# Optimization experiments

Measured on AMD Instinct MI355X. Metric: run time of the kernel, lower is better.

The kernel has to match this reference:

```python
import jax, jax.numpy as jnp
import numpy as np

D = 1024      # d_model
FFN = 4096    # encoder_ffn_dim
INTER = 4096  # intermediate_size (per-expert extra width)
E = 4         # num_experts
S = 3         # num_datasets
NH = 16       # attention heads
HD = D // NH
B = 4
L = 1024


def _ln(x, g, b, eps=1e-5):
    m = x.mean(-1, keepdims=True)
    v = ((x - m) ** 2).mean(-1, keepdims=True)
    return (x - m) / jnp.sqrt(v + eps) * g + b


def setup_inputs() -> dict:
    key = jax.random.key(0)
    keys = iter(jax.random.split(key, 32))

    def w(shape):
        return jax.random.normal(next(keys), shape, dtype=jnp.float32) * 0.02

    inp = {}
    inp["hidden_states"] = jax.random.normal(next(keys), (B, L, D), dtype=jnp.float32)
    inp["attention_mask"] = jnp.zeros((B, 1, L, L), jnp.float32)
    inp["layer_head_mask"] = jnp.ones((NH,), jnp.float32)
    inp["idxes"] = jax.random.randint(next(keys), (B,), 0, S, dtype=jnp.int32)
    for name, shape in [("q_w", (D, D)), ("k_w", (D, D)), ("v_w", (D, D)), ("o_w", (D, D)),
                        ("fc1_w", (FFN, D)), ("fc2_w", (D, FFN)),
                        ("exp_fc1_w", (E, INTER, D)), ("exp_fc2_w", (E, D, INTER)),
                        ("gate_w", (S, E, D))]:
        inp[name] = w(shape)
    for name, shape in [("q_b", (D,)), ("k_b", (D,)), ("v_b", (D,)), ("o_b", (D,)),
                        ("fc1_b", (FFN,)), ("fc2_b", (D,)),
                        ("exp_fc1_b", (E, INTER)), ("gate_b", (S, E))]:
        inp[name] = jnp.zeros(shape, jnp.float32)
    inp["ln1_g"] = jnp.ones((D,), jnp.float32)
    inp["ln1_b"] = jnp.zeros((D,), jnp.float32)
    inp["ln2_g"] = jnp.ones((D,), jnp.float32)
    inp["ln2_b"] = jnp.zeros((D,), jnp.float32)
    return inp


def reference(hidden_states, attention_mask, layer_head_mask, idxes,
              q_w, q_b, k_w, k_b, v_w, v_b, o_w, o_b,
              ln1_g, ln1_b, fc1_w, fc1_b, fc2_w, fc2_b,
              exp_fc1_w, exp_fc1_b, exp_fc2_w, gate_w, gate_b,
              ln2_g, ln2_b):
    Bb, Ll, Dm = hidden_states.shape
    residual = hidden_states
    scale = HD ** -0.5

    def heads(t):  # [B,L,D] -> [B,NH,L,HD]
        return t.reshape(Bb, Ll, NH, HD).transpose(0, 2, 1, 3)

    q = heads(hidden_states @ q_w.T + q_b) * scale
    k = heads(hidden_states @ k_w.T + k_b)
    v = heads(hidden_states @ v_w.T + v_b)
    scores = jnp.einsum('bhqd,bhkd->bhqk', q, k) + attention_mask  # [B,NH,L,L]
    probs = jax.nn.softmax(scores, axis=-1) * layer_head_mask[None, :, None, None]
    attn = jnp.einsum('bhqk,bhkd->bhqd', probs, v).transpose(0, 2, 1, 3).reshape(Bb, Ll, Dm)
    h = residual + attn @ o_w.T + o_b
    h = _ln(h, ln1_g, ln1_b)

    # --- MoE feed-forward (token-level top-1 routing, per-dataset gates) ---
    x = h.reshape(-1, Dm)                 # [T, D]
    ds = jnp.repeat(idxes, Ll)            # [T] dataset id per token
    Wg = gate_w[ds]                       # [T, E, D]
    logits = jnp.einsum('td,ted->te', x, Wg) + gate_b[ds]
    gp = jax.nn.softmax(logits, axis=-1)
    gate_value = gp.max(-1)               # [T]
    gate_idx = gp.argmax(-1)              # [T]

    out = jnp.zeros_like(x)
    for e in range(E):  # small fixed expert count
        W1 = jnp.concatenate([fc1_w, exp_fc1_w[e]], axis=0)     # [FFN+INTER, D]
        b1 = jnp.concatenate([fc1_b, exp_fc1_b[e]], axis=0)
        W2 = jnp.concatenate([fc2_w, exp_fc2_w[e]], axis=1)     # [D, FFN+INTER]
        hh = jax.nn.gelu(x @ W1.T + b1, approximate=False)
        y = hh @ W2.T + fc2_b
        y = _ln(x + y, ln2_g, ln2_b)
        out = out + jnp.where(gate_idx == e, gate_value, 0.0)[:, None] * y
    return out.reshape(Bb, Ll, Dm)
```

## Files before the change

kernel.cpp:

```cpp
#include <hip/hip_runtime.h>
#include <cstdint>
#include <cstddef>

#define DEV __device__ __forceinline__

typedef __bf16 bf16;
typedef __bf16 bf16x8 __attribute__((ext_vector_type(8)));
typedef __bf16 bf16x4v __attribute__((ext_vector_type(4)));
typedef float  f32x4  __attribute__((ext_vector_type(4)));

static constexpr int D_   = 1024;
static constexpr int FFN_ = 4096;
static constexpr int NH_  = 16;
static constexpr int HD_  = 64;
static constexpr int SEQ_ = 1024;
static constexpr int T_   = 4 * SEQ_;
static constexpr float L2E_ = 1.4426950408889634f;

DEV float gelu_f(float x) { return 0.5f * x * (1.f + erff(x * 0.70710678118654752f)); }

template<int N>
DEV float ror16(float x) {
  int i = __builtin_bit_cast(int, x);
  int r = __builtin_amdgcn_update_dpp(i, i, 0x120 + N, 0xf, 0xf, false);
  return __builtin_bit_cast(float, r);
}
DEV float rowMax16(float x) {
  x = fmaxf(x, ror16<8>(x)); x = fmaxf(x, ror16<4>(x));
  x = fmaxf(x, ror16<2>(x)); x = fmaxf(x, ror16<1>(x));
  return x;
}
DEV float rowSum16(float x) {
  x += ror16<8>(x); x += ror16<4>(x); x += ror16<2>(x); x += ror16<1>(x);
  return x;
}

__global__ __launch_bounds__(256) void k_cvt4(const float* __restrict__ a, const float* __restrict__ b,
                                              const float* __restrict__ c, const float* __restrict__ d,
                                              bf16* __restrict__ dst)
{
  size_t i = ((size_t)blockIdx.x * 256 + threadIdx.x) * 4;
  constexpr size_t M1 = 4ull << 20, M2 = 20ull << 20, M3 = 24ull << 20, M4 = 40ull << 20;
  const float* src; size_t si;
  if (i < M1)      { src = a; si = i; }
  else if (i < M2) { src = b; si = i - M1; }
  else if (i < M3) { src = c; si = i - M2; }
  else if (i < M4) { src = d; si = i - M3; }
  else return;
  float4 v = *(const float4*)(src + si);
  bf16x4v o;
  o[0] = (bf16)v.x; o[1] = (bf16)v.y; o[2] = (bf16)v.z; o[3] = (bf16)v.w;
  *(bf16x4v*)(dst + i) = o;
}

__global__ __launch_bounds__(256) void k_cvt_split_all(
    const float* __restrict__ h, const float* __restrict__ qw, const float* __restrict__ kw,
    const float* __restrict__ vw, const float* __restrict__ ow, bf16* __restrict__ out)
{
  int i = (blockIdx.x * 256 + threadIdx.x) * 4;
  if (i >= (8 << 20)) return;
  int seg = i >> 20;
  const float* src; int si;
  if (seg < 4)       { src = h;  si = i; }
  else if (seg == 4) { src = qw; si = i - (4 << 20); }
  else if (seg == 5) { src = kw; si = i - (5 << 20); }
  else if (seg == 6) { src = vw; si = i - (6 << 20); }
  else               { src = ow; si = i - (7 << 20); }
  float4 v = *(const float4*)(src + si);
  int r = i >> 10, c = i & 1023;
  bf16* base = out + (size_t)r * 2048 + c;
  float xs[4] = {v.x, v.y, v.z, v.w};
  #pragma unroll
  for (int j = 0; j < 4; ++j) {
    float x = xs[j];
    bf16 hi = (bf16)x;
    bf16 lo = (bf16)(x - (float)hi);
    base[j]        = hi;
    base[1024 + j] = lo;
  }
}

enum { EPI_QKV = 0, EPI_OPROJ, EPI_FF1, EPI_FF2 };

DEV int map_akt(int kt, bool split) { return split ? (kt < 64 ? kt : kt - 64) : kt; }
DEV int map_bkt(int kt, bool split) { return split ? (kt < 32 ? kt : kt - 32) : kt; }

template<int EPI, bool SPLIT, int TM, int TN>
__global__ __launch_bounds__(256)
void k_gemm(const bf16* __restrict__ A, const bf16* __restrict__ Bw,
            const float* __restrict__ bias, const float* __restrict__ bias2,
            const float* __restrict__ bias3, const float* __restrict__ resid,
            float* __restrict__ outF, bf16* __restrict__ outB,
            bf16* __restrict__ o2, bf16* __restrict__ o3,
            const int* __restrict__ perm, const int* __restrict__ seg,
            int Kphys, int nk, float scale)
{
  constexpr bool FUSED = (EPI == EPI_FF1 || EPI == EPI_FF2);
  constexpr int  NCOL  = (EPI == EPI_FF1) ? 4096 : 1024;
  constexpr int  SBX   = 4096 / TM;
  constexpr int  MF    = (TN == 128) ? (TM / 32) : (TM / 64);
  constexpr int  AISS  = TM / 64;
  constexpr int  BISS  = TN / 64;

  __shared__ __align__(16) bf16 sA[2][TM * 32];
  __shared__ __align__(16) bf16 sB[2][TN * 32];

  const int tid  = threadIdx.x;
  const int lane = tid & 63;
  const int w    = tid >> 6;
  const int lr   = lane & 15, kg = lane >> 4;
  const int wmBase = (TN == 128) ? (w >> 1) * (TM / 2) : w * (TM / 4);
  const int wnBase = (TN == 128) ? (w & 1) * 64 : 0;
  const int bx = blockIdx.x, by = blockIdx.y;

  const bool expertBlk = FUSED && (bx >= SBX);
  int e = 0;
  if (FUSED && expertBlk) { int r0 = (bx - SBX) * TM; while (e < 3 && r0 >= seg[e + 1]) e++; }
  const bf16* Bp = Bw + (expertBlk ? (size_t)(e + 1) * NCOL * Kphys : 0);

  size_t kOff = 0;
  if constexpr (EPI == EPI_FF2) kOff = (size_t)blockIdx.z * nk * 32;

  const bf16* aSrc[AISS]; const bf16* bSrc[BISS];
  #pragma unroll
  for (int i = 0; i < AISS; ++i) {
    int c = tid + i * 256;
    int koff = (c & 3) * 8;
    if (EPI == EPI_FF1 && expertBlk) {
      int pr = perm[(bx - SBX) * TM + (c >> 2)];
      aSrc[i] = A + (size_t)(pr < 0 ? 0 : pr) * Kphys + koff + kOff;
    } else {
      aSrc[i] = A + (size_t)(bx * TM + (c >> 2)) * Kphys + koff + kOff;
    }
  }
  #pragma unroll
  for (int i = 0; i < BISS; ++i) {
    int c = tid + i * 256;
    int koff = (c & 3) * 8;
    bSrc[i] = Bp + (size_t)(by * TN + (c >> 2)) * Kphys + koff + kOff;
  }

  f32x4 acc[MF][4] = {};

  #pragma unroll
  for (int i = 0; i < AISS; ++i)
    __builtin_amdgcn_global_load_lds((const void*)aSrc[i], (void*)((char*)sA[0] + (tid + i * 256) * 16), 16, 0, 0);
  #pragma unroll
  for (int i = 0; i < BISS; ++i)
    __builtin_amdgcn_global_load_lds((const void*)bSrc[i], (void*)((char*)sB[0] + (tid + i * 256) * 16), 16, 0, 0);
  __syncthreads();

  for (int kt = 0; kt < nk; ++kt) {
    const int cur = kt & 1;
    if (kt + 1 < nk) {
      int ak = map_akt(kt + 1, SPLIT), bk = map_bkt(kt + 1, SPLIT);
      #pragma unroll
      for (int i = 0; i < AISS; ++i)
        __builtin_amdgcn_global_load_lds((const void*)(aSrc[i] + (size_t)ak * 32),
                                         (void*)((char*)sA[cur ^ 1] + (tid + i * 256) * 16), 16, 0, 0);
      #pragma unroll
      for (int i = 0; i < BISS; ++i)
        __builtin_amdgcn_global_load_lds((const void*)(bSrc[i] + (size_t)bk * 32),
                                         (void*)((char*)sB[cur ^ 1] + (tid + i * 256) * 16), 16, 0, 0);
    }
    bf16x8 af[MF], bfr[4];
    #pragma unroll
    for (int m = 0; m < MF; ++m)
      af[m] = *(const bf16x8*)&sA[cur][(wmBase + m * 16 + lr) * 32 + kg * 8];
    #pragma unroll
    for (int n = 0; n < 4; ++n)
      bfr[n] = *(const bf16x8*)&sB[cur][(wnBase + n * 16 + lr) * 32 + kg * 8];
    #pragma unroll
    for (int m = 0; m < MF; ++m)
      #pragma unroll
      for (int n = 0; n < 4; ++n)
        acc[m][n] = __builtin_amdgcn_mfma_f32_16x16x32_bf16(af[m], bfr[n], acc[m][n], 0, 0, 0);
    __syncthreads();
  }

  #pragma unroll
  for (int m = 0; m < MF; ++m) {
    #pragma unroll
    for (int n = 0; n < 4; ++n) {
      int gc = by * TN + wnBase + n * 16 + lr;
      #pragma unroll
      for (int r = 0; r < 4; ++r) {
        int row = bx * TM + wmBase + m * 16 + kg * 4 + r;
        float v = acc[m][n][r];
        if constexpr (EPI == EPI_QKV) {
          const int which = by >> 3;
          const int wcol = gc & 1023;
          int bq = row >> 10, li = row & 1023, hh = wcol >> 6, d = wcol & 63;
          if (which == 0) {
            float y = (v + bias[wcol]) * scale;
            bf16* base = outB + ((size_t)(bq * NH_ + hh) * SEQ_ + li) * 128 + d;
            bf16 hi = (bf16)y, lo = (bf16)(y - (float)hi);
            base[0] = hi; base[64] = lo;
          } else if (which == 1) {
            float y = v + bias2[wcol];
            bf16* base = o2 + ((size_t)(bq * NH_ + hh) * SEQ_ + li) * 128 + d;
            bf16 hi = (bf16)y, lo = (bf16)(y - (float)hi);
            base[0] = hi; base[64] = lo;
          } else {
            float y = v + bias3[wcol];
            bf16* base = o3 + ((size_t)(bq * NH_ + hh) * HD_ + d) * 2048 + li;
            bf16 hi = (bf16)y, lo = (bf16)(y - (float)hi);
            base[0] = hi; base[1024] = lo;
          }
        } else if constexpr (EPI == EPI_OPROJ) {
          size_t idx = (size_t)row * 1024 + gc;
          outF[idx] = v + bias[gc] + resid[idx];
        } else if constexpr (EPI == EPI_FF1) {
          float y = v + (expertBlk ? bias2[e * 4096 + gc] : bias[gc]);
          outB[(size_t)row * 4096 + gc] = (bf16)gelu_f(y);
        } else if constexpr (EPI == EPI_FF2) {
          o2[((size_t)blockIdx.z * 8704 + row) * 1024 + gc] = (bf16)v;
        }
      }
    }
  }
}

__global__ __launch_bounds__(256)
void k_attn(const bf16* __restrict__ q2, const bf16* __restrict__ k2,
            const bf16* __restrict__ vT2, const float* __restrict__ mask,
            const float* __restrict__ lhm, bf16* __restrict__ ctx2)
{
  const int blk = (blockIdx.x & 7) * 128 + (blockIdx.x >> 3);
  const int bh = blk >> 4, qt4 = blk & 15;
  const int tid = threadIdx.x;
  const int w = tid >> 6;
  const int lane = tid & 63, lr = lane & 15, kg = lane >> 4;
  const int b = bh >> 4, h = bh & 15;
  const int q0 = (qt4 * 4 + w) * 16;

  __shared__ __align__(16) bf16 sK[2][4096];
  __shared__ __align__(16) bf16 sV[2][4096];
  __shared__ __align__(16) float Pb[4][16][32];
  float (*P)[32] = Pb[w];

  const bf16* qp = q2 + ((size_t)bh * SEQ_ + q0) * 128;
  bf16x8 aq0 = *(const bf16x8*)(qp + (size_t)lr * 128 +  0 + kg * 8);
  bf16x8 aq1 = *(const bf16x8*)(qp + (size_t)lr * 128 + 32 + kg * 8);
  bf16x8 aq2 = *(const bf16x8*)(qp + (size_t)lr * 128 + 64 + kg * 8);
  bf16x8 aq3 = *(const bf16x8*)(qp + (size_t)lr * 128 + 96 + kg * 8);

  const bf16* kp = k2 + (size_t)bh * SEQ_ * 128;
  const bf16* vp = vT2 + (size_t)bh * HD_ * 2048;
  const float* mp = mask + ((size_t)b * SEQ_ + q0) * SEQ_;

  auto stage = [&](int buf, int kb) {
    #pragma unroll
    for (int i = 0; i < 2; ++i) {
      int c = i * 256 + w * 64 + lane;
      int cs = c ^ ((c >> 4) & 7);
      __builtin_amdgcn_global_load_lds((const void*)(kp + (size_t)kb * 128 + cs * 8),
                                       (void*)&sK[buf][(size_t)(i * 256 + w * 64) * 8], 16, 0, 0);
      int d = c >> 3, p = (c & 7) ^ (d & 7);
      const bf16* vsrc = vp + (size_t)d * 2048 + (p < 4 ? kb + p * 8 : 1024 + kb + (p - 4) * 8);
      __builtin_amdgcn_global_load_lds((const void*)vsrc,
                                       (void*)&sV[buf][(size_t)(i * 256 + w * 64) * 8], 16, 0, 0);
    }
  };

  float m_run[4], l_run[4];
  f32x4 o[4] = {};
  #pragma unroll
  for (int r = 0; r < 4; ++r) { m_run[r] = -1e30f; l_run[r] = 0.f; }

  float mreg[8];
  #pragma unroll
  for (int n = 0; n < 2; ++n)
    #pragma unroll
    for (int r = 0; r < 4; ++r)
      mreg[n * 4 + r] = mp[(size_t)(kg * 4 + r) * SEQ_ + n * 16 + lr];

  stage(0, 0);
  __syncthreads();

  for (int kc = 0; kc < SEQ_ / 32; ++kc) {
    const int kb = kc * 32;
    const int cur = kc & 1;
    if (kc + 1 < SEQ_ / 32) stage(cur ^ 1, kb + 32);

    const char* kbase = (const char*)sK[cur];
    const char* vbase = (const char*)sV[cur];

    f32x4 s[2];
    #pragma unroll
    for (int n = 0; n < 2; ++n) {
      f32x4 t = {0.f, 0.f, 0.f, 0.f};
      int key = n * 16 + lr;
      int rowb = (key << 8) + (kg << 4);
      int sw = (key & 7) << 4;
      bf16x8 bk0 = *(const bf16x8*)(kbase + ((rowb +   0) ^ sw));
      bf16x8 bk1 = *(const bf16x8*)(kbase + ((rowb +  64) ^ sw));
      bf16x8 bk2 = *(const bf16x8*)(kbase + ((rowb + 128) ^ sw));
      bf16x8 bk3 = *(const bf16x8*)(kbase + ((rowb + 192) ^ sw));
      t = __builtin_amdgcn_mfma_f32_16x16x32_bf16(aq0, bk0, t, 0, 0, 0);
      t = __builtin_amdgcn_mfma_f32_16x16x32_bf16(aq1, bk1, t, 0, 0, 0);
      t = __builtin_amdgcn_mfma_f32_16x16x32_bf16(aq2, bk0, t, 0, 0, 0);
      t = __builtin_amdgcn_mfma_f32_16x16x32_bf16(aq3, bk1, t, 0, 0, 0);
      t = __builtin_amdgcn_mfma_f32_16x16x32_bf16(aq0, bk2, t, 0, 0, 0);
      t = __builtin_amdgcn_mfma_f32_16x16x32_bf16(aq1, bk3, t, 0, 0, 0);
      s[n] = t;
    }
    #pragma unroll
    for (int n = 0; n < 2; ++n)
      #pragma unroll
      for (int r = 0; r < 4; ++r)
        s[n][r] = fmaf(mreg[n * 4 + r], L2E_, s[n][r]);
    if (kc + 1 < SEQ_ / 32) {
      #pragma unroll
      for (int n = 0; n < 2; ++n)
        #pragma unroll
        for (int r = 0; r < 4; ++r)
          mreg[n * 4 + r] = mp[(size_t)(kg * 4 + r) * SEQ_ + kb + 32 + n * 16 + lr];
    }

    float cm[4], mnew[4], alpha[4], rs[4], pv[2][4];
    #pragma unroll
    for (int r = 0; r < 4; ++r) cm[r] = rowMax16(fmaxf(s[0][r], s[1][r]));
    #pragma unroll
    for (int r = 0; r < 4; ++r) { mnew[r] = fmaxf(m_run[r], cm[r]); alpha[r] = exp2f(m_run[r] - mnew[r]); }
    #pragma unroll
    for (int n = 0; n < 2; ++n)
      #pragma unroll
      for (int r = 0; r < 4; ++r) pv[n][r] = exp2f(s[n][r] - mnew[r]);
    #pragma unroll
    for (int r = 0; r < 4; ++r) rs[r] = rowSum16(pv[0][r] + pv[1][r]);
    #pragma unroll
    for (int r = 0; r < 4; ++r) { l_run[r] = l_run[r] * alpha[r] + rs[r]; m_run[r] = mnew[r]; }
    #pragma unroll
    for (int n = 0; n < 4; ++n)
      #pragma unroll
      for (int r = 0; r < 4; ++r) o[n][r] *= alpha[r];

    #pragma unroll
    for (int n = 0; n < 2; ++n)
      #pragma unroll
      for (int r = 0; r < 4; ++r) {
        int row = kg * 4 + r, col = n * 16 + lr;
        int cg = (col >> 2) ^ (row & 7);
        P[row][(cg << 2) | (col & 3)] = pv[n][r];
      }
    asm volatile("s_waitcnt lgkmcnt(0)" ::: "memory");
    __builtin_amdgcn_sched_barrier(0);

    f32x4 pA = *(const f32x4*)&P[lr][((kg * 2) ^ (lr & 7)) << 2];
    f32x4 pB = *(const f32x4*)&P[lr][((kg * 2 + 1) ^ (lr & 7)) << 2];
    bf16x8 ph, pl;
    #pragma unroll
    for (int j = 0; j < 4; ++j) {
      ph[j] = (bf16)pA[j]; pl[j] = (bf16)(pA[j] - (float)ph[j]);
      ph[4 + j] = (bf16)pB[j]; pl[4 + j] = (bf16)(pB[j] - (float)ph[4 + j]);
    }

    #pragma unroll
    for (int n = 0; n < 4; ++n) {
      int d = n * 16 + lr;
      int rowb = (d << 7) + (kg << 4);
      int sw = (d & 7) << 4;
      bf16x8 bvh = *(const bf16x8*)(vbase + ((rowb +  0) ^ sw));
      bf16x8 bvl = *(const bf16x8*)(vbase + ((rowb + 64) ^ sw));
      o[n] = __builtin_amdgcn_mfma_f32_16x16x32_bf16(ph, bvh, o[n], 0, 0, 0);
      o[n] = __builtin_amdgcn_mfma_f32_16x16x32_bf16(pl, bvh, o[n], 0, 0, 0);
      o[n] = __builtin_amdgcn_mfma_f32_16x16x32_bf16(ph, bvl, o[n], 0, 0, 0);
    }

    __syncthreads();
  }

  const float hm = lhm[h];
  #pragma unroll
  for (int r = 0; r < 4; ++r) {
    float rln = hm / l_run[r];
    #pragma unroll
    for (int n = 0; n < 4; ++n) {
      int li = q0 + kg * 4 + r;
      int col = h * HD_ + n * 16 + lr;
      float y = o[n][r] * rln;
      bf16* base = ctx2 + ((size_t)b * SEQ_ + li) * 2048;
      bf16 hi = (bf16)y, lo = (bf16)(y - (float)hi);
      base[col] = hi; base[1024 + col] = lo;
    }
  }
}

DEV float blockReduceSum(float v, int tid, float* sm)
{
  #pragma unroll
  for (int d = 1; d < 64; d <<= 1) v += __shfl_xor(v, d, 64);
  if ((tid & 63) == 0) sm[tid >> 6] = v;
  __syncthreads();
  float r = sm[0] + sm[1] + sm[2] + sm[3];
  __syncthreads();
  return r;
}

__global__ __launch_bounds__(256)
void k_ln1gate(const float* __restrict__ hpre, const float* __restrict__ gam, const float* __restrict__ bet,
               const float* __restrict__ gw, const float* __restrict__ gb, const int* __restrict__ idxes,
               float* __restrict__ h, bf16* __restrict__ hb,
               float* __restrict__ gv, int* __restrict__ gi)
{
  __shared__ float sm[4];
  __shared__ float red[4][4];
  int t = blockIdx.x, tid = threadIdx.x;
  const float* x = hpre + (size_t)t * 1024;
  float4 v = *(const float4*)(x + tid * 4);
  float mean = blockReduceSum(v.x + v.y + v.z + v.w, tid, sm) * (1.f / 1024.f);
  float d0 = v.x - mean, d1 = v.y - mean, d2 = v.z - mean, d3 = v.w - mean;
  float var = blockReduceSum(d0*d0 + d1*d1 + d2*d2 + d3*d3, tid, sm) * (1.f / 1024.f);
  float inv = rsqrtf(var + 1e-5f);
  float4 g4 = *(const float4*)(gam + tid * 4);
  float4 b4 = *(const float4*)(bet + tid * 4);
  float y0 = d0 * inv * g4.x + b4.x, y1 = d1 * inv * g4.y + b4.y;
  float y2 = d2 * inv * g4.z + b4.z, y3 = d3 * inv * g4.w + b4.w;
  float4 yo; yo.x = y0; yo.y = y1; yo.z = y2; yo.w = y3;
  *(float4*)(h + (size_t)t * 1024 + tid * 4) = yo;
  bf16x4v hv; hv[0] = (bf16)y0; hv[1] = (bf16)y1; hv[2] = (bf16)y2; hv[3] = (bf16)y3;
  *(bf16x4v*)(hb + (size_t)t * 1024 + tid * 4) = hv;

  int ds = idxes[t >> 10];
  const float* wg = gw + (size_t)ds * 4096;
  float a[4];
  #pragma unroll
  for (int e = 0; e < 4; ++e) {
    float4 wv = *(const float4*)(wg + e * 1024 + tid * 4);
    a[e] = y0 * wv.x + y1 * wv.y + y2 * wv.z + y3 * wv.w;
  }
  int lane = tid & 63, wid = tid >> 6;
  #pragma unroll
  for (int e = 0; e < 4; ++e) {
    float vv = a[e];
    #pragma unroll
    for (int d = 1; d < 64; d <<= 1) vv += __shfl_xor(vv, d, 64);
    if (lane == 0) red[wid][e] = vv;
  }
  __syncthreads();
  if (tid == 0) {
    float lg[4];
    #pragma unroll
    for (int e = 0; e < 4; ++e) lg[e] = red[0][e] + red[1][e] + red[2][e] + red[3][e] + gb[ds * 4 + e];
    int best = 0; float bv = lg[0];
    #pragma unroll
    for (int e = 1; e < 4; ++e) if (lg[e] > bv) { bv = lg[e]; best = e; }
    float se = 0.f;
    #pragma unroll
    for (int e = 0; e < 4; ++e) se += expf(lg[e] - bv);
    gv[t] = 1.f / se;
    gi[t] = best;
  }
}

__global__ __launch_bounds__(1024)
void k_route_all(const int* __restrict__ gi, int* __restrict__ meta,
                 int* __restrict__ perm, int* __restrict__ inv)
{
  __shared__ int cnt[4], seg[5], cur[4];
  int tid = threadIdx.x;
  if (tid < 4) { cnt[tid] = 0; cur[tid] = 0; }
  __syncthreads();
  #pragma unroll
  for (int k = 0; k < 4; ++k) atomicAdd(&cnt[gi[tid + k * 1024]], 1);
  #pragma unroll
  for (int k = 0; k < 5; ++k) { int i = tid + k * 1024; if (i < 4608) perm[i] = -1; }
  __syncthreads();
  if (tid == 0) {
    int s = 0;
    #pragma unroll
    for (int e = 0; e < 4; ++e) { seg[e] = s; s += (cnt[e] + 127) & ~127; }
    seg[4] = s;
    #pragma unroll
    for (int e = 0; e < 5; ++e) meta[8 + e] = seg[e];
  }
  __syncthreads();
  #pragma unroll
  for (int k = 0; k < 4; ++k) {
    int t = tid + k * 1024;
    int e = gi[t];
    int p = atomicAdd(&cur[e], 1);
    int rowp = seg[e] + p;
    perm[rowp] = t;
    inv[t] = rowp;
  }
}

__global__ __launch_bounds__(256)
void k_final(const float* __restrict__ h, const bf16* __restrict__ P,
             const float* __restrict__ b2, const float* __restrict__ gam,
             const float* __restrict__ bet, const float* __restrict__ gv,
             const int* __restrict__ inv, float* __restrict__ out)
{
  __shared__ float sm[4];
  int t = blockIdx.x, tid = threadIdx.x;
  constexpr size_t CH = 8704ull * 1024ull;
  int er = 4096 + inv[t];
  bf16x4v q0 = *(const bf16x4v*)(P + (size_t)t * 1024 + tid * 4);
  bf16x4v q1 = *(const bf16x4v*)(P + CH + (size_t)t * 1024 + tid * 4);
  bf16x4v q2 = *(const bf16x4v*)(P + (size_t)er * 1024 + tid * 4);
  bf16x4v q3 = *(const bf16x4v*)(P + CH + (size_t)er * 1024 + tid * 4);
  float4 a = *(const float4*)(h + (size_t)t * 1024 + tid * 4);
  float4 bb = *(const float4*)(b2 + tid * 4);
  float z0 = a.x + (float)q0[0] + (float)q1[0] + (float)q2[0] + (float)q3[0] + bb.x;
  float z1 = a.y + (float)q0[1] + (float)q1[1] + (float)q2[1] + (float)q3[1] + bb.y;
  float z2 = a.z + (float)q0[2] + (float)q1[2] + (float)q2[2] + (float)q3[2] + bb.z;
  float z3 = a.w + (float)q0[3] + (float)q1[3] + (float)q2[3] + (float)q3[3] + bb.w;
  float mean = blockReduceSum(z0 + z1 + z2 + z3, tid, sm) * (1.f / 1024.f);
  float d0 = z0 - mean, d1 = z1 - mean, d2 = z2 - mean, d3 = z3 - mean;
  float var = blockReduceSum(d0*d0 + d1*d1 + d2*d2 + d3*d3, tid, sm) * (1.f / 1024.f);
  float invd = rsqrtf(var + 1e-5f);
  float4 g4 = *(const float4*)(gam + tid * 4);
  float4 b4 = *(const float4*)(bet + tid * 4);
  float gval = gv[t];
  float4 r;
  r.x = gval * (d0 * invd * g4.x + b4.x);
  r.y = gval * (d1 * invd * g4.y + b4.y);
  r.z = gval * (d2 * invd * g4.z + b4.z);
  r.w = gval * (d3 * invd * g4.w + b4.w);
  *(float4*)(out + (size_t)t * 1024 + tid * 4) = r;
}

extern "C" void kernel_launch(void* const* d_in, const int* in_sizes, int n_in,
                              void* d_out, int out_size, void* d_ws, size_t ws_size,
                              hipStream_t stream)
{
  const float* hidden = (const float*)d_in[0];
  const float* mask   = (const float*)d_in[1];
  const float* lhm    = (const float*)d_in[2];
  const int*   idxes  = (const int*)d_in[3];
  const float* qw = (const float*)d_in[4];
  const float* kw = (const float*)d_in[5];
  const float* vw = (const float*)d_in[6];
  const float* ow = (const float*)d_in[7];
  const float* fc1w  = (const float*)d_in[8];
  const float* fc2w  = (const float*)d_in[9];
  const float* efc1w = (const float*)d_in[10];
  const float* efc2w = (const float*)d_in[11];
  const float* gatew = (const float*)d_in[12];
  const float* qb = (const float*)d_in[13];
  const float* kb = (const float*)d_in[14];
  const float* vb = (const float*)d_in[15];
  const float* ob = (const float*)d_in[16];
  const float* fc1b  = (const float*)d_in[17];
  const float* fc2b  = (const float*)d_in[18];
  const float* efc1b = (const float*)d_in[19];
  const float* gateb = (const float*)d_in[20];
  const float* ln1g = (const float*)d_in[21];
  const float* ln1b = (const float*)d_in[22];
  const float* ln2g = (const float*)d_in[23];
  const float* ln2b = (const float*)d_in[24];
  float* out = (float*)d_out;
  char* ws = (char*)d_ws;

  constexpr size_t MB = 1024ull * 1024ull;
  constexpr size_t O_H    = 0;
  constexpr size_t O_HBF  = O_H + 16 * MB;
  constexpr size_t O_GV   = O_HBF + 8 * MB;
  constexpr size_t O_GI   = O_GV + 16 * 1024;
  constexpr size_t O_PERM = O_GI + 16 * 1024;
  constexpr size_t O_META = O_PERM + 18432;
  constexpr size_t O_INV  = O_META + 256;
  constexpr size_t O_U    = (O_INV + 16384 + 255) & ~255ull;
  constexpr size_t O_X2   = O_U;
  constexpr size_t O_WQ2  = O_X2 + 16 * MB;
  constexpr size_t O_Q2   = O_WQ2 + 16 * MB;
  constexpr size_t O_K2   = O_Q2 + 16 * MB;
  constexpr size_t O_VT2  = O_K2 + 16 * MB;
  constexpr size_t O_CTX2 = O_VT2 + 16 * MB;
  constexpr size_t O_HPRE = O_CTX2 + 16 * MB;
  constexpr size_t O_WO2  = O_WQ2 + 12 * MB;
  constexpr size_t O_W1B  = O_U;
  constexpr size_t O_WE1B = O_W1B + 8 * MB;
  constexpr size_t O_W2B  = O_WE1B + 32 * MB;
  constexpr size_t O_WE2B = O_W2B + 8 * MB;
  constexpr size_t O_HHS  = O_WE2B + 32 * MB;
  constexpr size_t O_HHE  = O_HHS + 32 * MB;
  constexpr size_t O_P    = O_HHE + 36 * MB;
  (void)ws_size; (void)in_sizes; (void)n_in; (void)out_size;

  dim3 blk(256);
  k_cvt_split_all<<<8192, 256, 0, stream>>>(hidden, qw, kw, vw, ow, (bf16*)(ws + O_X2));

  const float qscale = 0.125f * L2E_;
  k_gemm<EPI_QKV, true, 128, 128><<<dim3(32, 24), blk, 0, stream>>>(
      (bf16*)(ws + O_X2), (bf16*)(ws + O_WQ2), qb, kb, vb, nullptr,
      nullptr, (bf16*)(ws + O_Q2), (bf16*)(ws + O_K2), (bf16*)(ws + O_VT2),
      nullptr, nullptr, 2048, 96, qscale);

  k_attn<<<1024, 256, 0, stream>>>((bf16*)(ws + O_Q2), (bf16*)(ws + O_K2), (bf16*)(ws + O_VT2),
                                   mask, lhm, (bf16*)(ws + O_CTX2));

  k_gemm<EPI_OPROJ, true, 128, 64><<<dim3(32, 16), blk, 0, stream>>>(
      (bf16*)(ws + O_CTX2), (bf16*)(ws + O_WO2), ob, nullptr, nullptr, hidden,
      (float*)(ws + O_HPRE), nullptr, nullptr, nullptr, nullptr, nullptr, 2048, 96, 1.0f);
  k_ln1gate<<<4096, 256, 0, stream>>>((float*)(ws + O_HPRE), ln1g, ln1b, gatew, gateb, idxes,
                                      (float*)(ws + O_H), (bf16*)(ws + O_HBF),
                                      (float*)(ws + O_GV), (int*)(ws + O_GI));

  k_cvt4<<<40960, 256, 0, stream>>>(fc1w, efc1w, fc2w, efc2w, (bf16*)(ws + O_W1B));
  k_route_all<<<1, 1024, 0, stream>>>((int*)(ws + O_GI), (int*)(ws + O_META),
                                      (int*)(ws + O_PERM), (int*)(ws + O_INV));

  k_gemm<EPI_FF1, false, 128, 128><<<dim3(68, 32), blk, 0, stream>>>(
      (bf16*)(ws + O_HBF), (bf16*)(ws + O_W1B), fc1b, efc1b, nullptr, nullptr,
      nullptr, (bf16*)(ws + O_HHS), nullptr, nullptr,
      (int*)(ws + O_PERM), (int*)(ws + O_META) + 8, 1024, 32, 1.0f);
  k_gemm<EPI_FF2, false, 128, 128><<<dim3(68, 8, 2), blk, 0, stream>>>(
      (bf16*)(ws + O_HHS), (bf16*)(ws + O_W2B), nullptr, nullptr, nullptr, nullptr,
      nullptr, nullptr, (bf16*)(ws + O_P), nullptr,
      nullptr, (int*)(ws + O_META) + 8, 4096, 64, 1.0f);

  k_final<<<4096, 256, 0, stream>>>((float*)(ws + O_H), (bf16*)(ws + O_P), fc2b, ln2g, ln2b,
                                    (float*)(ws + O_GV), (int*)(ws + O_INV), out);
}
```

Measured before the change: 603.3 us.

## Split-K the output projection and swap erf GELU for a sigmoid approximation

The output projection GEMM is split along K into two z-slices. Each slice writes raw fp32 partials, and the LayerNorm/gate kernel sums the two partials with the residual and the o_proj bias before normalising. This doubles the block count of a small 512-block GEMM to improve CU occupancy, at the cost of extra partial-buffer traffic. The exact erf GELU in the FF1 epilogue is also replaced by a sigmoid-form tanh approximation using exp2 and a fast reciprocal. This cuts transcendental cost but is a numerical approximation of approximate=False GELU. The O_HPRE buffer must now hold two full partial planes.

```diff
diff --git a/kernel.cpp b/kernel.cpp
--- a/kernel.cpp
+++ b/kernel.cpp
@@ -17,7 +17,10 @@
 static constexpr int T_   = 4 * SEQ_;
 static constexpr float L2E_ = 1.4426950408889634f;
 
-DEV float gelu_f(float x) { return 0.5f * x * (1.f + erff(x * 0.70710678118654752f)); }
+DEV float gelu_f(float x) {
+  float g2 = x * fmaf(-0.102944f, x * x, -2.302212f);
+  return x * __builtin_amdgcn_rcpf(1.f + exp2f(g2));
+}
 
 template<int N>
 DEV float ror16(float x) {
@@ -112,14 +115,12 @@
   const int wmBase = (TN == 128) ? (w >> 1) * (TM / 2) : w * (TM / 4);
   const int wnBase = (TN == 128) ? (w & 1) * 64 : 0;
   const int bx = blockIdx.x, by = blockIdx.y;
+  const int ktBase = (EPI == EPI_OPROJ || EPI == EPI_FF2) ? blockIdx.z * nk : 0;
 
   const bool expertBlk = FUSED && (bx >= SBX);
   int e = 0;
   if (FUSED && expertBlk) { int r0 = (bx - SBX) * TM; while (e < 3 && r0 >= seg[e + 1]) e++; }
   const bf16* Bp = Bw + (expertBlk ? (size_t)(e + 1) * NCOL * Kphys : 0);
-
-  size_t kOff = 0;
-  if constexpr (EPI == EPI_FF2) kOff = (size_t)blockIdx.z * nk * 32;
 
   const bf16* aSrc[AISS]; const bf16* bSrc[BISS];
   #pragma unroll
@@ -128,32 +129,37 @@
     int koff = (c & 3) * 8;
     if (EPI == EPI_FF1 && expertBlk) {
       int pr = perm[(bx - SBX) * TM + (c >> 2)];
-      aSrc[i] = A + (size_t)(pr < 0 ? 0 : pr) * Kphys + koff + kOff;
+      aSrc[i] = A + (size_t)(pr < 0 ? 0 : pr) * Kphys + koff;
     } else {
-      aSrc[i] = A + (size_t)(bx * TM + (c >> 2)) * Kphys + koff + kOff;
+      aSrc[i] = A + (size_t)(bx * TM + (c >> 2)) * Kphys + koff;
     }
   }
   #pragma unroll
   for (int i = 0; i < BISS; ++i) {
     int c = tid + i * 256;
     int koff = (c & 3) * 8;
-    bSrc[i] = Bp + (size_t)(by * TN + (c >> 2)) * Kphys + koff + kOff;
+    bSrc[i] = Bp + (size_t)(by * TN + (c >> 2)) * Kphys + koff;
   }
 
   f32x4 acc[MF][4] = {};
 
-  #pragma unroll
-  for (int i = 0; i < AISS; ++i)
-    __builtin_amdgcn_global_load_lds((const void*)aSrc[i], (void*)((char*)sA[0] + (tid + i * 256) * 16), 16, 0, 0);
-  #pragma unroll
-  for (int i = 0; i < BISS; ++i)
-    __builtin_amdgcn_global_load_lds((const void*)bSrc[i], (void*)((char*)sB[0] + (tid + i * 256) * 16), 16, 0, 0);
+  {
+    int ak0 = map_akt(ktBase, SPLIT), bk0 = map_bkt(ktBase, SPLIT);
+    #pragma unroll
+    for (int i = 0; i < AISS; ++i)
+      __builtin_amdgcn_global_load_lds((const void*)(aSrc[i] + (size_t)ak0 * 32),
+                                       (void*)((char*)sA[0] + (tid + i * 256) * 16), 16, 0, 0);
+    #pragma unroll
+    for (int i = 0; i < BISS; ++i)
+      __builtin_amdgcn_global_load_lds((const void*)(bSrc[i] + (size_t)bk0 * 32),
+                                       (void*)((char*)sB[0] + (tid + i * 256) * 16), 16, 0, 0);
+  }
   __syncthreads();
 
   for (int kt = 0; kt < nk; ++kt) {
     const int cur = kt & 1;
     if (kt + 1 < nk) {
-      int ak = map_akt(kt + 1, SPLIT), bk = map_bkt(kt + 1, SPLIT);
+      int ak = map_akt(ktBase + kt + 1, SPLIT), bk = map_bkt(ktBase + kt + 1, SPLIT);
       #pragma unroll
       for (int i = 0; i < AISS; ++i)
         __builtin_amdgcn_global_load_lds((const void*)(aSrc[i] + (size_t)ak * 32),
@@ -208,8 +214,7 @@
             base[0] = hi; base[1024] = lo;
           }
         } else if constexpr (EPI == EPI_OPROJ) {
-          size_t idx = (size_t)row * 1024 + gc;
-          outF[idx] = v + bias[gc] + resid[idx];
+          outF[((size_t)blockIdx.z * 4096 + row) * 1024 + gc] = v;
         } else if constexpr (EPI == EPI_FF1) {
           float y = v + (expertBlk ? bias2[e * 4096 + gc] : bias[gc]);
           outB[(size_t)row * 4096 + gc] = (bf16)gelu_f(y);
@@ -399,7 +404,8 @@
 }
 
 __global__ __launch_bounds__(256)
-void k_ln1gate(const float* __restrict__ hpre, const float* __restrict__ gam, const float* __restrict__ bet,
+void k_ln1gate(const float* __restrict__ resid, const float* __restrict__ Pp, const float* __restrict__ ob,
+               const float* __restrict__ gam, const float* __restrict__ bet,
                const float* __restrict__ gw, const float* __restrict__ gb, const int* __restrict__ idxes,
                float* __restrict__ h, bf16* __restrict__ hb,
                float* __restrict__ gv, int* __restrict__ gi)
@@ -407,10 +413,17 @@
   __shared__ float sm[4];
   __shared__ float red[4][4];
   int t = blockIdx.x, tid = threadIdx.x;
-  const float* x = hpre + (size_t)t * 1024;
-  float4 v = *(const float4*)(x + tid * 4);
-  float mean = blockReduceSum(v.x + v.y + v.z + v.w, tid, sm) * (1.f / 1024.f);
-  float d0 = v.x - mean, d1 = v.y - mean, d2 = v.z - mean, d3 = v.w - mean;
+  constexpr size_t CH = 4096ull * 1024ull;
+  float4 rv = *(const float4*)(resid + (size_t)t * 1024 + tid * 4);
+  float4 p0 = *(const float4*)(Pp + (size_t)t * 1024 + tid * 4);
+  float4 p1 = *(const float4*)(Pp + CH + (size_t)t * 1024 + tid * 4);
+  float4 bo = *(const float4*)(ob + tid * 4);
+  float z0 = rv.x + p0.x + p1.x + bo.x;
+  float z1 = rv.y + p0.y + p1.y + bo.y;
+  float z2 = rv.z + p0.z + p1.z + bo.z;
+  float z3 = rv.w + p0.w + p1.w + bo.w;
+  float mean = blockReduceSum(z0 + z1 + z2 + z3, tid, sm) * (1.f / 1024.f);
+  float d0 = z0 - mean, d1 = z1 - mean, d2 = z2 - mean, d3 = z3 - mean;
   float var = blockReduceSum(d0*d0 + d1*d1 + d2*d2 + d3*d3, tid, sm) * (1.f / 1024.f);
   float inv = rsqrtf(var + 1e-5f);
   float4 g4 = *(const float4*)(gam + tid * 4);
@@ -592,10 +605,11 @@
   k_attn<<<1024, 256, 0, stream>>>((bf16*)(ws + O_Q2), (bf16*)(ws + O_K2), (bf16*)(ws + O_VT2),
                                    mask, lhm, (bf16*)(ws + O_CTX2));
 
-  k_gemm<EPI_OPROJ, true, 128, 64><<<dim3(32, 16), blk, 0, stream>>>(
-      (bf16*)(ws + O_CTX2), (bf16*)(ws + O_WO2), ob, nullptr, nullptr, hidden,
-      (float*)(ws + O_HPRE), nullptr, nullptr, nullptr, nullptr, nullptr, 2048, 96, 1.0f);
-  k_ln1gate<<<4096, 256, 0, stream>>>((float*)(ws + O_HPRE), ln1g, ln1b, gatew, gateb, idxes,
+  k_gemm<EPI_OPROJ, true, 128, 64><<<dim3(32, 16, 2), blk, 0, stream>>>(
+      (bf16*)(ws + O_CTX2), (bf16*)(ws + O_WO2), nullptr, nullptr, nullptr, nullptr,
+      (float*)(ws + O_HPRE), nullptr, nullptr, nullptr, nullptr, nullptr, 2048, 48, 1.0f);
+  k_ln1gate<<<4096, 256, 0, stream>>>(hidden, (float*)(ws + O_HPRE), ob, ln1g, ln1b,
+                                      gatew, gateb, idxes,
                                       (float*)(ws + O_H), (bf16*)(ws + O_HBF),
                                       (float*)(ws + O_GV), (int*)(ws + O_GI));
 
```

After: 570.8 us. -5.4%, faster.
